# Kernel tuning notes

Measured on AMD Instinct MI355X. Metric: run time of the kernel, lower is better.

The kernel has to match this reference:

```python
import jax, jax.numpy as jnp
import numpy as np

SEG = 4      # segment_size
H = 8        # n_heads
D = 1024     # d_model
B = 8
S = 4096


def setup_inputs() -> dict:
    key = jax.random.key(0)
    ks = jax.random.split(key, 9)
    s = 0.02  # init scale for weights
    return {
        "x": jax.random.normal(ks[0], (B, S, D), dtype=jnp.float32),
        "proj_qk_w": jax.random.normal(ks[1], (D, D), dtype=jnp.float32) * s,
        "proj_qk_b": jax.random.normal(ks[2], (D,), dtype=jnp.float32) * s,
        "proj_v_w": jax.random.normal(ks[3], (D, D), dtype=jnp.float32) * s,
        "proj_v_b": jax.random.normal(ks[4], (D,), dtype=jnp.float32) * s,
        "in_proj_w": jax.random.normal(ks[5], (3 * D, D), dtype=jnp.float32) * s,
        "in_proj_b": jax.random.normal(ks[6], (3 * D,), dtype=jnp.float32) * s,
        "out_proj_w": jax.random.normal(ks[7], (D, D), dtype=jnp.float32) * s,
        "out_proj_b": jax.random.normal(ks[8], (D,), dtype=jnp.float32) * s,
    }


def reference(x, proj_qk_w, proj_qk_b, proj_v_w, proj_v_b,
              in_proj_w, in_proj_b, out_proj_w, out_proj_b):
    b, seq_len, d = x.shape
    hd = d // H
    # torch: pad = seg - S % seg  (pads a full segment when S % seg == 0)
    pad = SEG - seq_len % SEG
    x = jnp.concatenate([x, x[:, :pad]], axis=1)          # [b, T, d]
    T = seq_len + pad
    a = T // SEG
    # cat(chunk(x, a, dim=1), dim=0): block-major stacking -> [a*b, SEG, d]
    xb = x.reshape(b, a, SEG, d).transpose(1, 0, 2, 3).reshape(a * b, SEG, d)

    # extra projections (same qk projection used for query and key)
    qk_in = xb @ proj_qk_w.T + proj_qk_b                   # [a*b, SEG, d]
    v_in = xb @ proj_v_w.T + proj_v_b

    # nn.MultiheadAttention in-projection
    wq, wk, wv = jnp.split(in_proj_w, 3, axis=0)
    bq, bk, bv = jnp.split(in_proj_b, 3)
    q = (qk_in @ wq.T + bq).reshape(a * b, SEG, H, hd)
    k = (qk_in @ wk.T + bk).reshape(a * b, SEG, H, hd)
    v = (v_in @ wv.T + bv).reshape(a * b, SEG, H, hd)

    scale = 1.0 / np.sqrt(hd).astype(np.float32)
    scores = jnp.einsum('nqhd,nkhd->nhqk', q * scale, k)   # [a*b, H, SEG, SEG]
    # diagonal exclusion mask (True on the diagonal = masked)
    diag = jnp.eye(SEG, dtype=bool)
    scores = jnp.where(diag[None, None], jnp.finfo(scores.dtype).min, scores)
    attn = jax.nn.softmax(scores, axis=-1)
    o = jnp.einsum('nhqk,nkhd->nqhd', attn, v).reshape(a * b, SEG, d)
    o = o @ out_proj_w.T + out_proj_b                      # [a*b, SEG, d]

    # cat(chunk(x, a, dim=0), dim=1): invert the block stacking
    out = o.reshape(a, b, SEG, d).transpose(1, 0, 2, 3).reshape(b, T, d)
    return out[:, :seq_len]
```

## Files before the change

kernel.cpp:

```cpp
#include <hip/hip_runtime.h>
#include <hip/hip_bf16.h>

typedef __bf16 bf16x8 __attribute__((ext_vector_type(8)));
typedef float f32x4 __attribute__((ext_vector_type(4)));

__device__ __forceinline__ float bf2f(unsigned int u) {
    unsigned int x = u << 16;
    return __builtin_bit_cast(float, x);
}
__device__ __forceinline__ unsigned short f2bf(float f) {
    unsigned int x = __builtin_bit_cast(unsigned int, f);
    x += 0x7fffu + ((x >> 16) & 1u);
    return (unsigned short)(x >> 16);
}

__device__ __forceinline__ void gld_lds16(const unsigned short* g, unsigned short* s) {
    __builtin_amdgcn_global_load_lds((const __attribute__((address_space(1))) void*)g,
                                     (__attribute__((address_space(3))) void*)s, 16, 0, 0);
}

template<bool OUT_F32>
__global__ __launch_bounds__(256) void gemm_bt(
    const unsigned short* __restrict__ A, int lda,
    const unsigned short* __restrict__ B,
    const float* __restrict__ bias,
    void* __restrict__ C, int N, int K)
{
    __shared__ unsigned short As[128 * 32];
    __shared__ unsigned short Bs[128 * 32];
    const int tid   = threadIdx.x;
    const int lane  = tid & 63;
    const int wave  = tid >> 6;
    const int wm    = (wave >> 1) * 64;
    const int wn    = (wave & 1) * 64;
    const int lrow  = lane & 15;
    const int lquad = lane >> 4;
    const long bm = (long)blockIdx.y * 128;
    const long bn = (long)blockIdx.x * 128;

    f32x4 acc[4][4];
#pragma unroll
    for (int i = 0; i < 4; i++)
#pragma unroll
        for (int j = 0; j < 4; j++)
            acc[i][j] = (f32x4){0.f, 0.f, 0.f, 0.f};

    const int r0 = tid >> 2;
    const int c0 = (tid & 3) * 8;
    const unsigned short* Ag0 = A + (bm + r0) * (long)lda + c0;
    const unsigned short* Ag1 = A + (bm + r0 + 64) * (long)lda + c0;
    const unsigned short* Bg0 = B + (bn + r0) * (long)K + c0;
    const unsigned short* Bg1 = B + (bn + r0 + 64) * (long)K + c0;
    unsigned short* As0 = &As[tid * 8];
    unsigned short* As1 = &As[tid * 8 + 2048];
    unsigned short* Bs0 = &Bs[tid * 8];
    unsigned short* Bs1 = &Bs[tid * 8 + 2048];

    for (int k0 = 0; k0 < K; k0 += 32) {
        gld_lds16(Ag0 + k0, As0);
        gld_lds16(Ag1 + k0, As1);
        gld_lds16(Bg0 + k0, Bs0);
        gld_lds16(Bg1 + k0, Bs1);
        __syncthreads();
        bf16x8 af[4], bq[4];
#pragma unroll
        for (int i = 0; i < 4; i++)
            af[i] = *(const bf16x8*)&As[(wm + i * 16 + lrow) * 32 + lquad * 8];
#pragma unroll
        for (int j = 0; j < 4; j++)
            bq[j] = *(const bf16x8*)&Bs[(wn + j * 16 + lrow) * 32 + lquad * 8];
#pragma unroll
        for (int i = 0; i < 4; i++)
#pragma unroll
            for (int j = 0; j < 4; j++)
                acc[i][j] = __builtin_amdgcn_mfma_f32_16x16x32_bf16(af[i], bq[j], acc[i][j], 0, 0, 0);
        __syncthreads();
    }

#pragma unroll
    for (int j = 0; j < 4; j++) {
        const int col = (int)bn + wn + j * 16 + lrow;
        const float bvv = bias ? bias[col] : 0.f;
#pragma unroll
        for (int i = 0; i < 4; i++) {
            const long rowb = bm + wm + i * 16 + lquad * 4;
#pragma unroll
            for (int r = 0; r < 4; r++) {
                float v = acc[i][j][r] + bvv;
                if (OUT_F32)
                    ((float*)C)[(rowb + r) * (long)N + col] = v;
                else
                    ((unsigned short*)C)[(rowb + r) * (long)N + col] = f2bf(v);
            }
        }
    }
}

__global__ __launch_bounds__(256) void attn4(
    const unsigned short* __restrict__ QKV,
    unsigned short* __restrict__ O)
{
    const int wave = threadIdx.x >> 6;
    const int lane = threadIdx.x & 63;
    const int gh = blockIdx.x * 4 + wave;
    const int g = gh >> 3, h = gh & 7;
    const long row0 = (long)g * 4;
    const int dof = h * 128 + lane * 2;
    const float scale = 0.08838834764831845f;

    float q[4][2], k[4][2], v[4][2];
#pragma unroll
    for (int i = 0; i < 4; i++) {
        const unsigned short* qr = QKV + (row0 + i) * 3072 + dof;
        unsigned int uq = *(const unsigned int*)qr;
        unsigned int uk = *(const unsigned int*)(qr + 1024);
        unsigned int uv = *(const unsigned int*)(qr + 2048);
        q[i][0] = bf2f(uq & 0xffffu); q[i][1] = bf2f(uq >> 16);
        k[i][0] = bf2f(uk & 0xffffu); k[i][1] = bf2f(uk >> 16);
        v[i][0] = bf2f(uv & 0xffffu); v[i][1] = bf2f(uv >> 16);
    }
    float s[4][4];
#pragma unroll
    for (int i = 0; i < 4; i++)
#pragma unroll
        for (int j = 0; j < 4; j++)
            s[i][j] = q[i][0] * k[j][0] + q[i][1] * k[j][1];
#pragma unroll
    for (int m = 1; m < 64; m <<= 1)
#pragma unroll
        for (int i = 0; i < 4; i++)
#pragma unroll
            for (int j = 0; j < 4; j++)
                s[i][j] += __shfl_xor(s[i][j], m, 64);

#pragma unroll
    for (int i = 0; i < 4; i++) {
        float mx = -3.0e38f;
#pragma unroll
        for (int j = 0; j < 4; j++)
            if (j != i) mx = fmaxf(mx, s[i][j] * scale);
        float p[4], den = 0.f;
#pragma unroll
        for (int j = 0; j < 4; j++) {
            p[j] = (j == i) ? 0.f : __expf(s[i][j] * scale - mx);
            den += p[j];
        }
        const float inv = 1.f / den;
        float o0 = 0.f, o1 = 0.f;
#pragma unroll
        for (int j = 0; j < 4; j++) {
            const float a = p[j] * inv;
            o0 += a * v[j][0];
            o1 += a * v[j][1];
        }
        unsigned int packed = (unsigned int)f2bf(o0) | ((unsigned int)f2bf(o1) << 16);
        *(unsigned int*)(O + (row0 + i) * 1024 + dof) = packed;
    }
}

__global__ __launch_bounds__(256) void cvt_bf16(const float* __restrict__ in,
                                                unsigned short* __restrict__ out, int n4)
{
    int i = blockIdx.x * blockDim.x + threadIdx.x;
    if (i >= n4) return;
    float4 v = ((const float4*)in)[i];
    unsigned int a = (unsigned int)f2bf(v.x) | ((unsigned int)f2bf(v.y) << 16);
    unsigned int b = (unsigned int)f2bf(v.z) | ((unsigned int)f2bf(v.w) << 16);
    ((uint2*)out)[i] = make_uint2(a, b);
}

__global__ __launch_bounds__(256) void transpose_cvt(const float* __restrict__ in,
                                                     unsigned short* __restrict__ out, int n)
{
    __shared__ unsigned short tile[64][65];
    const int bx = blockIdx.x * 64, by = blockIdx.y * 64;
    const int tx = threadIdx.x & 63, ty = threadIdx.x >> 6;
    for (int r = ty; r < 64; r += 4)
        tile[r][tx] = f2bf(in[(long)(by + r) * n + bx + tx]);
    __syncthreads();
    for (int r = ty; r < 64; r += 4)
        out[(long)(bx + r) * n + by + tx] = tile[tx][r];
}

__global__ __launch_bounds__(256) void bias_prep(const float* __restrict__ win,
                                                 const float* __restrict__ bqk,
                                                 const float* __restrict__ bv,
                                                 const float* __restrict__ bin,
                                                 float* __restrict__ bbig)
{
    const int row = blockIdx.x * 4 + (threadIdx.x >> 6);
    const int lane = threadIdx.x & 63;
    const float* b = (row < 2048) ? bqk : bv;
    float s = 0.f;
    for (int t = lane; t < 1024; t += 64) s += win[(long)row * 1024 + t] * b[t];
#pragma unroll
    for (int m = 1; m < 64; m <<= 1) s += __shfl_xor(s, m, 64);
    if (lane == 0) bbig[row] = s + bin[row];
}

extern "C" void kernel_launch(void* const* d_in, const int* in_sizes, int n_in,
                              void* d_out, int out_size, void* d_ws, size_t ws_size,
                              hipStream_t stream)
{
    (void)in_sizes; (void)n_in; (void)out_size; (void)ws_size;
    const float* x    = (const float*)d_in[0];
    const float* wqk  = (const float*)d_in[1];
    const float* bqk  = (const float*)d_in[2];
    const float* wv   = (const float*)d_in[3];
    const float* bv   = (const float*)d_in[4];
    const float* win  = (const float*)d_in[5];
    const float* bin  = (const float*)d_in[6];
    const float* wout = (const float*)d_in[7];
    const float* bout = (const float*)d_in[8];

    char* ws = (char*)d_ws;
    unsigned short* buf0  = (unsigned short*)ws;
    unsigned short* qkv   = (unsigned short*)(ws + (64ll << 20));
    unsigned short* win16 = (unsigned short*)(ws + (256ll << 20));
    unsigned short* wqkT  = (unsigned short*)(ws + (262ll << 20));
    unsigned short* wvT   = (unsigned short*)(ws + (264ll << 20));
    unsigned short* wbig  = (unsigned short*)(ws + (266ll << 20));
    unsigned short* wo16  = (unsigned short*)(ws + (272ll << 20));
    float*          bbig  = (float*)(ws + (274ll << 20));
    unsigned short* o16   = buf0;

    dim3 blk(256);
    cvt_bf16<<<32768, 256, 0, stream>>>(x, buf0, 8388608);
    cvt_bf16<<<3072, 256, 0, stream>>>(win, win16, 786432);
    cvt_bf16<<<1024, 256, 0, stream>>>(wout, wo16, 262144);
    transpose_cvt<<<dim3(16, 16), blk, 0, stream>>>(wqk, wqkT, 1024);
    transpose_cvt<<<dim3(16, 16), blk, 0, stream>>>(wv, wvT, 1024);
    bias_prep<<<768, blk, 0, stream>>>(win, bqk, bv, bin, bbig);

    gemm_bt<false><<<dim3(8, 16), blk, 0, stream>>>(win16, 1024, wqkT, nullptr,
                                                    wbig, 1024, 1024);
    gemm_bt<false><<<dim3(8, 8), blk, 0, stream>>>(win16 + 2048ll * 1024, 1024, wvT, nullptr,
                                                   wbig + 2048ll * 1024, 1024, 1024);

    gemm_bt<false><<<dim3(24, 256), blk, 0, stream>>>(buf0, 1024, wbig, bbig, qkv, 3072, 1024);

    attn4<<<16384, blk, 0, stream>>>(qkv, o16);

    gemm_bt<true><<<dim3(8, 256), blk, 0, stream>>>(o16, 1024, wo16, bout, d_out, 1024, 1024);
}
```

Before: 743.8 us.

## Vectorize GEMM epilogue via swapped MFMA operands, widen attention loads, merge prep launches

The GEMM now swaps MFMA operands so each lane holds four consecutive output columns, which lets the epilogue write float4/uint2 vectors and read bias as float4 instead of doing scalar strided stores. The attention kernel handles one head per half-wave with 8-byte loads and stores, and its shuffle reduction drops from six steps to five. Weight conversions, the two transposes and the two weight-fusion GEMMs are each merged into one launch, with a B-pointer split inside the GEMM. This cuts store instruction count and launch overhead, and requires the bias pointer to be 16-byte aligned.

Result: faster. 729.1 us (-2.0%).

```diff
diff --git a/kernel.cpp b/kernel.cpp
--- a/kernel.cpp
+++ b/kernel.cpp
@@ -23,6 +23,7 @@
 __global__ __launch_bounds__(256) void gemm_bt(
     const unsigned short* __restrict__ A, int lda,
     const unsigned short* __restrict__ B,
+    const unsigned short* __restrict__ B2, long bsplit,
     const float* __restrict__ bias,
     void* __restrict__ C, int N, int K)
 {
@@ -37,6 +38,7 @@
     const int lquad = lane >> 4;
     const long bm = (long)blockIdx.y * 128;
     const long bn = (long)blockIdx.x * 128;
+    const unsigned short* Bp = (bm >= bsplit) ? B2 : B;
 
     f32x4 acc[4][4];
 #pragma unroll
@@ -49,8 +51,8 @@
     const int c0 = (tid & 3) * 8;
     const unsigned short* Ag0 = A + (bm + r0) * (long)lda + c0;
     const unsigned short* Ag1 = A + (bm + r0 + 64) * (long)lda + c0;
-    const unsigned short* Bg0 = B + (bn + r0) * (long)K + c0;
-    const unsigned short* Bg1 = B + (bn + r0 + 64) * (long)K + c0;
+    const unsigned short* Bg0 = Bp + (bn + r0) * (long)K + c0;
+    const unsigned short* Bg1 = Bp + (bn + r0 + 64) * (long)K + c0;
     unsigned short* As0 = &As[tid * 8];
     unsigned short* As1 = &As[tid * 8 + 2048];
     unsigned short* Bs0 = &Bs[tid * 8];
@@ -73,24 +75,28 @@
         for (int i = 0; i < 4; i++)
 #pragma unroll
             for (int j = 0; j < 4; j++)
-                acc[i][j] = __builtin_amdgcn_mfma_f32_16x16x32_bf16(af[i], bq[j], acc[i][j], 0, 0, 0);
+                acc[i][j] = __builtin_amdgcn_mfma_f32_16x16x32_bf16(bq[j], af[i], acc[i][j], 0, 0, 0);
         __syncthreads();
     }
 
 #pragma unroll
-    for (int j = 0; j < 4; j++) {
-        const int col = (int)bn + wn + j * 16 + lrow;
-        const float bvv = bias ? bias[col] : 0.f;
-#pragma unroll
-        for (int i = 0; i < 4; i++) {
-            const long rowb = bm + wm + i * 16 + lquad * 4;
-#pragma unroll
-            for (int r = 0; r < 4; r++) {
-                float v = acc[i][j][r] + bvv;
-                if (OUT_F32)
-                    ((float*)C)[(rowb + r) * (long)N + col] = v;
-                else
-                    ((unsigned short*)C)[(rowb + r) * (long)N + col] = f2bf(v);
+    for (int i = 0; i < 4; i++) {
+        const long row = bm + wm + i * 16 + lrow;
+#pragma unroll
+        for (int j = 0; j < 4; j++) {
+            const int colb = (int)bn + wn + j * 16 + lquad * 4;
+            float4 b4 = bias ? ((const float4*)bias)[colb >> 2]
+                             : make_float4(0.f, 0.f, 0.f, 0.f);
+            const float v0 = acc[i][j][0] + b4.x;
+            const float v1 = acc[i][j][1] + b4.y;
+            const float v2 = acc[i][j][2] + b4.z;
+            const float v3 = acc[i][j][3] + b4.w;
+            if (OUT_F32) {
+                *(float4*)&((float*)C)[row * (long)N + colb] = make_float4(v0, v1, v2, v3);
+            } else {
+                unsigned int lo = (unsigned int)f2bf(v0) | ((unsigned int)f2bf(v1) << 16);
+                unsigned int hi = (unsigned int)f2bf(v2) | ((unsigned int)f2bf(v3) << 16);
+                *(uint2*)&((unsigned short*)C)[row * (long)N + colb] = make_uint2(lo, hi);
             }
         }
     }
@@ -102,31 +108,37 @@
 {
     const int wave = threadIdx.x >> 6;
     const int lane = threadIdx.x & 63;
-    const int gh = blockIdx.x * 4 + wave;
+    const int half = lane >> 5;
+    const int l    = lane & 31;
+    const int gh = blockIdx.x * 8 + wave * 2 + half;
     const int g = gh >> 3, h = gh & 7;
     const long row0 = (long)g * 4;
-    const int dof = h * 128 + lane * 2;
+    const int d0 = h * 128 + l * 4;
     const float scale = 0.08838834764831845f;
 
-    float q[4][2], k[4][2], v[4][2];
+    float q[4][4], k[4][4], v[4][4];
 #pragma unroll
     for (int i = 0; i < 4; i++) {
-        const unsigned short* qr = QKV + (row0 + i) * 3072 + dof;
-        unsigned int uq = *(const unsigned int*)qr;
-        unsigned int uk = *(const unsigned int*)(qr + 1024);
-        unsigned int uv = *(const unsigned int*)(qr + 2048);
-        q[i][0] = bf2f(uq & 0xffffu); q[i][1] = bf2f(uq >> 16);
-        k[i][0] = bf2f(uk & 0xffffu); k[i][1] = bf2f(uk >> 16);
-        v[i][0] = bf2f(uv & 0xffffu); v[i][1] = bf2f(uv >> 16);
+        const unsigned short* base = QKV + (row0 + i) * 3072 + d0;
+        uint2 uq = *(const uint2*)base;
+        uint2 uk = *(const uint2*)(base + 1024);
+        uint2 uv = *(const uint2*)(base + 2048);
+        q[i][0] = bf2f(uq.x & 0xffffu); q[i][1] = bf2f(uq.x >> 16);
+        q[i][2] = bf2f(uq.y & 0xffffu); q[i][3] = bf2f(uq.y >> 16);
+        k[i][0] = bf2f(uk.x & 0xffffu); k[i][1] = bf2f(uk.x >> 16);
+        k[i][2] = bf2f(uk.y & 0xffffu); k[i][3] = bf2f(uk.y >> 16);
+        v[i][0] = bf2f(uv.x & 0xffffu); v[i][1] = bf2f(uv.x >> 16);
+        v[i][2] = bf2f(uv.y & 0xffffu); v[i][3] = bf2f(uv.y >> 16);
     }
     float s[4][4];
 #pragma unroll
     for (int i = 0; i < 4; i++)
 #pragma unroll
         for (int j = 0; j < 4; j++)
-            s[i][j] = q[i][0] * k[j][0] + q[i][1] * k[j][1];
-#pragma unroll
-    for (int m = 1; m < 64; m <<= 1)
+            s[i][j] = q[i][0] * k[j][0] + q[i][1] * k[j][1]
+                    + q[i][2] * k[j][2] + q[i][3] * k[j][3];
+#pragma unroll
+    for (int m = 1; m < 32; m <<= 1)
 #pragma unroll
         for (int i = 0; i < 4; i++)
 #pragma unroll
@@ -146,15 +158,16 @@
             den += p[j];
         }
         const float inv = 1.f / den;
-        float o0 = 0.f, o1 = 0.f;
+        float o0 = 0.f, o1 = 0.f, o2 = 0.f, o3 = 0.f;
 #pragma unroll
         for (int j = 0; j < 4; j++) {
             const float a = p[j] * inv;
-            o0 += a * v[j][0];
-            o1 += a * v[j][1];
+            o0 += a * v[j][0]; o1 += a * v[j][1];
+            o2 += a * v[j][2]; o3 += a * v[j][3];
         }
-        unsigned int packed = (unsigned int)f2bf(o0) | ((unsigned int)f2bf(o1) << 16);
-        *(unsigned int*)(O + (row0 + i) * 1024 + dof) = packed;
+        unsigned int lo = (unsigned int)f2bf(o0) | ((unsigned int)f2bf(o1) << 16);
+        unsigned int hi = (unsigned int)f2bf(o2) | ((unsigned int)f2bf(o3) << 16);
+        *(uint2*)(O + (row0 + i) * 1024 + d0) = make_uint2(lo, hi);
     }
 }
 
@@ -169,9 +182,30 @@
     ((uint2*)out)[i] = make_uint2(a, b);
 }
 
-__global__ __launch_bounds__(256) void transpose_cvt(const float* __restrict__ in,
-                                                     unsigned short* __restrict__ out, int n)
-{
+__global__ __launch_bounds__(256) void cvt_weights(const float* __restrict__ win,
+                                                   unsigned short* __restrict__ win16,
+                                                   const float* __restrict__ wout,
+                                                   unsigned short* __restrict__ wo16)
+{
+    int i = blockIdx.x * blockDim.x + threadIdx.x;
+    const float* in;
+    unsigned short* out;
+    int j;
+    if (i < 786432) { in = win; out = win16; j = i; }
+    else            { in = wout; out = wo16; j = i - 786432; }
+    float4 v = ((const float4*)in)[j];
+    unsigned int a = (unsigned int)f2bf(v.x) | ((unsigned int)f2bf(v.y) << 16);
+    unsigned int b = (unsigned int)f2bf(v.z) | ((unsigned int)f2bf(v.w) << 16);
+    ((uint2*)out)[j] = make_uint2(a, b);
+}
+
+__global__ __launch_bounds__(256) void transpose_cvt2(const float* __restrict__ a,
+                                                      unsigned short* __restrict__ oa,
+                                                      const float* __restrict__ b,
+                                                      unsigned short* __restrict__ ob, int n)
+{
+    const float* in = blockIdx.z ? b : a;
+    unsigned short* out = blockIdx.z ? ob : oa;
     __shared__ unsigned short tile[64][65];
     const int bx = blockIdx.x * 64, by = blockIdx.y * 64;
     const int tx = threadIdx.x & 63, ty = threadIdx.x >> 6;
@@ -223,23 +257,22 @@
     unsigned short* wo16  = (unsigned short*)(ws + (272ll << 20));
     float*          bbig  = (float*)(ws + (274ll << 20));
     unsigned short* o16   = buf0;
+    const long NOSPLIT = 1ll << 40;
 
     dim3 blk(256);
     cvt_bf16<<<32768, 256, 0, stream>>>(x, buf0, 8388608);
-    cvt_bf16<<<3072, 256, 0, stream>>>(win, win16, 786432);
-    cvt_bf16<<<1024, 256, 0, stream>>>(wout, wo16, 262144);
-    transpose_cvt<<<dim3(16, 16), blk, 0, stream>>>(wqk, wqkT, 1024);
-    transpose_cvt<<<dim3(16, 16), blk, 0, stream>>>(wv, wvT, 1024);
+    cvt_weights<<<4096, 256, 0, stream>>>(win, win16, wout, wo16);
+    transpose_cvt2<<<dim3(16, 16, 2), blk, 0, stream>>>(wqk, wqkT, wv, wvT, 1024);
     bias_prep<<<768, blk, 0, stream>>>(win, bqk, bv, bin, bbig);
 
-    gemm_bt<false><<<dim3(8, 16), blk, 0, stream>>>(win16, 1024, wqkT, nullptr,
-                                                    wbig, 1024, 1024);
-    gemm_bt<false><<<dim3(8, 8), blk, 0, stream>>>(win16 + 2048ll * 1024, 1024, wvT, nullptr,
-                                                   wbig + 2048ll * 1024, 1024, 1024);
-
-    gemm_bt<false><<<dim3(24, 256), blk, 0, stream>>>(buf0, 1024, wbig, bbig, qkv, 3072, 1024);
-
-    attn4<<<16384, blk, 0, stream>>>(qkv, o16);
-
-    gemm_bt<true><<<dim3(8, 256), blk, 0, stream>>>(o16, 1024, wo16, bout, d_out, 1024, 1024);
-}
+    gemm_bt<false><<<dim3(8, 24), blk, 0, stream>>>(win16, 1024, wqkT, wvT, 2048,
+                                                    nullptr, wbig, 1024, 1024);
+
+    gemm_bt<false><<<dim3(24, 256), blk, 0, stream>>>(buf0, 1024, wbig, wbig, NOSPLIT,
+                                                      bbig, qkv, 3072, 1024);
+
+    attn4<<<8192, blk, 0, stream>>>(qkv, o16);
+
+    gemm_bt<true><<<dim3(8, 256), blk, 0, stream>>>(o16, 1024, wo16, wo16, NOSPLIT,
+                                                    bout, d_out, 1024, 1024);
+}
```
